# Kernel optimization log

Measured on AMD Instinct MI355X. Metric: run time of the kernel, lower is better.

## Reference

```python
import jax, jax.numpy as jnp
import numpy as np

HEADS = 16

def setup_inputs() -> dict:
    key = jax.random.key(0)
    ks = jax.random.split(key, 7)
    B, S, E = 2, 2048, 1024
    return {
        "query": jax.random.normal(ks[0], (B, S, E), dtype=jnp.float32),
        "key": jax.random.normal(ks[1], (B, S, E), dtype=jnp.float32),
        "value": jax.random.normal(ks[2], (B, S, E), dtype=jnp.float32),
        "Wqkv": jax.random.normal(ks[3], (E, 3 * E), dtype=jnp.float32) * (E ** -0.5),
        "bqkv": jax.random.normal(ks[4], (3 * E,), dtype=jnp.float32) * 0.02,
        "Wproj": jax.random.normal(ks[5], (E, E), dtype=jnp.float32) * (E ** -0.5),
        "bproj": jax.random.normal(ks[6], (E,), dtype=jnp.float32) * 0.02,
    }

def reference(query, key, value, Wqkv, bqkv, Wproj, bproj):
    # key/value args are unused in the original forward (overwritten by QKV split)
    B, S, E = query.shape
    H = HEADS
    hd = E // H
    qkv = query @ Wqkv + bqkv                     # [B, S, 3E]
    qkv = qkv.reshape(B, S, H, 3 * hd).transpose(0, 2, 1, 3)  # [B, H, S, 3hd]
    q = qkv[..., :hd]
    k = qkv[..., hd:2 * hd]
    v = qkv[..., 2 * hd:]
    qk = jnp.einsum("bhqd,bhkd->bhqk", q, k)
    # faithful quirk: original divides by head_dim**-0.5, i.e. multiplies by sqrt(hd)
    scaled = qk / (hd ** -0.5)
    attn = jax.nn.softmax(scaled, axis=-1)        # dropout p=0 -> identity
    out = jnp.einsum("bhqk,bhkd->bhqd", attn, v)  # [B, H, S, hd]
    out = out.transpose(0, 2, 1, 3).reshape(B, S, E)
    return out @ Wproj + bproj
```

## Files before the change

### kernel.cpp

```cpp
#include <hip/hip_runtime.h>
#include <hip/hip_bf16.h>
#include <stdint.h>

typedef __attribute__((ext_vector_type(8))) _Float16 f16x8;
typedef __attribute__((ext_vector_type(4))) _Float16 f16x4;
typedef __attribute__((ext_vector_type(4))) float f32x4;

static constexpr int BATCH = 2;
static constexpr int SEQ = 2048;
static constexpr int EMB = 1024;
static constexpr int NH = 16;
static constexpr int HD_ = 64;

#define AS1 __attribute__((address_space(1)))
#define AS3 __attribute__((address_space(3)))

__device__ __forceinline__ void gload_lds16(const void* g, void* l) {
  __builtin_amdgcn_global_load_lds((const AS1 uint32_t*)g, (AS3 uint32_t*)l, 16, 0, 0);
}

__device__ __forceinline__ f32x4 mfma16(f16x8 a, f16x8 b, f32x4 c) {
  return __builtin_amdgcn_mfma_f32_16x16x32_f16(a, b, c, 0, 0, 0);
}

__device__ __forceinline__ f16x8 swzread(const _Float16* base, int row, int blk) {
  return *(const f16x8*)((const char*)base + row * 128 +
                         ((blk * 16) ^ ((row & 7) << 4)));
}

__global__ __launch_bounds__(256) void k_prep(const float* __restrict__ q,
                                              _Float16* __restrict__ qo,
                                              const float* __restrict__ wqkv,
                                              _Float16* __restrict__ wqkvo,
                                              const float* __restrict__ wproj,
                                              _Float16* __restrict__ wprojo) {
  __shared__ float tile[32][33];
  const int blk = blockIdx.x;
  const int t = threadIdx.x;
  if (blk < 4096) {
    const int idx = blk * 256 + t;
    float4 v = reinterpret_cast<const float4*>(q)[idx];
    const float* f = reinterpret_cast<const float*>(&v);
    _Float16 h[4];
#pragma unroll
    for (int i = 0; i < 4; ++i) h[i] = (_Float16)f[i];
    reinterpret_cast<uint2*>(qo)[idx] = *reinterpret_cast<uint2*>(h);
    return;
  }
  const float* in;
  _Float16* out;
  int R, C, bx, by;
  bool perm;
  if (blk < 4096 + 3072) {
    const int lo = blk - 4096;
    bx = lo % 96;
    by = lo / 96;
    in = wqkv; out = wqkvo; R = 1024; C = 3072; perm = true;
  } else {
    const int lo = blk - 7168;
    bx = lo & 31;
    by = lo >> 5;
    in = wproj; out = wprojo; R = 1024; C = 1024; perm = false;
  }
  const int tr = t >> 5, tc = t & 31;
  const int r0 = by * 32, c0 = bx * 32;
#pragma unroll
  for (int rr = 0; rr < 32; rr += 8)
    tile[tr + rr][tc] = in[(size_t)(r0 + tr + rr) * C + c0 + tc];
  __syncthreads();
#pragma unroll
  for (int rr = 0; rr < 32; rr += 8) {
    const int c = c0 + tr + rr;
    int d = c;
    if (perm) {
      const int h = c / 192, r = c - h * 192;
      d = (r < 64) ? h * 64 + r
                   : (r < 128 ? 1024 + h * 64 + (r - 64) : 2048 + h * 64 + (r - 128));
    }
    out[(size_t)d * R + r0 + tc] = (_Float16)tile[tc][tr + rr];
  }
}

__global__ __launch_bounds__(256) void k_gemm_qkv(const _Float16* __restrict__ A,
                                                  const _Float16* __restrict__ Bt,
                                                  const float* __restrict__ bias,
                                                  _Float16* __restrict__ oq,
                                                  _Float16* __restrict__ ok,
                                                  _Float16* __restrict__ ov) {
  constexpr int K = EMB;
  __shared__ _Float16 As[2][128 * 32];
  __shared__ _Float16 Bs[2][128 * 32];
  const int t = threadIdx.x;
  const int l = t & 63, w = t >> 6;
  const int lr = l & 15, lg = l >> 4;
  const int wr = w >> 1, wc = w & 1;
  const int id = blockIdx.x;
  const int xcd = id & 7, wg = id >> 3;
  const int m0 = (xcd * 4 + wg / 24) * 128;
  const int n0 = (wg % 24) * 128;

  auto stage = [&](int buf, int k0) {
#pragma unroll
    for (int j = 0; j < 2; ++j) {
      const int c = t + 256 * j;
      const int row = c >> 2, cb = c & 3;
      gload_lds16(A + (size_t)(m0 + row) * K + k0 + cb * 8, &As[buf][c * 8]);
      gload_lds16(Bt + (size_t)(n0 + row) * K + k0 + cb * 8, &Bs[buf][c * 8]);
    }
  };

  f32x4 acc[4][4];
#pragma unroll
  for (int m = 0; m < 4; ++m)
#pragma unroll
    for (int n = 0; n < 4; ++n) acc[m][n] = f32x4{0.f, 0.f, 0.f, 0.f};

  stage(0, 0);
  const int NT = K / 32;
  int cur = 0;
  for (int kt = 0; kt < NT; ++kt) {
    __syncthreads();
    if (kt + 1 < NT) stage(cur ^ 1, (kt + 1) * 32);
    f16x8 af[4], bf[4];
#pragma unroll
    for (int m = 0; m < 4; ++m)
      af[m] = *(const f16x8*)&As[cur][(wr * 64 + m * 16 + lr) * 32 + lg * 8];
#pragma unroll
    for (int n = 0; n < 4; ++n)
      bf[n] = *(const f16x8*)&Bs[cur][(wc * 64 + n * 16 + lr) * 32 + lg * 8];
#pragma unroll
    for (int m = 0; m < 4; ++m)
#pragma unroll
      for (int n = 0; n < 4; ++n) acc[m][n] = mfma16(af[m], bf[n], acc[m][n]);
    cur ^= 1;
  }

  const int sec = n0 >> 10;
#pragma unroll
  for (int m = 0; m < 4; ++m) {
#pragma unroll
    for (int n = 0; n < 4; ++n) {
      const int col = n0 + wc * 64 + n * 16 + lr;
      const int cc = col & 1023;
      const int h = cc >> 6, r = cc & 63;
      const float bv = bias[h * 192 + sec * 64 + r];
      const int row0 = m0 + wr * 64 + m * 16 + lg * 4;
      const int b = row0 >> 11, s0 = row0 & (SEQ - 1);
      if (sec == 2) {
        f16x4 vv;
#pragma unroll
        for (int i = 0; i < 4; ++i) vv[i] = (_Float16)(acc[m][n][i] + bv);
        *(f16x4*)&ov[(((size_t)b * NH + h) * HD_ + r) * SEQ + s0] = vv;
      } else {
#pragma unroll
        for (int i = 0; i < 4; ++i) {
          const float v = acc[m][n][i] + bv;
          const size_t dst = (((size_t)b * NH + h) * SEQ + s0 + i) * HD_ + r;
          if (sec == 0)
            oq[dst] = (_Float16)(v * 11.5415603f);
          else
            ok[dst] = (_Float16)v;
        }
      }
    }
  }
}

__global__ __launch_bounds__(256) void k_gemm_proj(const _Float16* __restrict__ A,
                                                   const _Float16* __restrict__ Bt,
                                                   const float* __restrict__ bias,
                                                   float* __restrict__ of) {
  constexpr int K = EMB, N = EMB;
  __shared__ _Float16 As[2][128 * 32];
  __shared__ _Float16 Bs[2][128 * 32];
  const int t = threadIdx.x;
  const int l = t & 63, w = t >> 6;
  const int lr = l & 15, lg = l >> 4;
  const int wr = w >> 1, wc = w & 1;
  const int m0 = blockIdx.y * 128, n0 = blockIdx.x * 128;

  auto stage = [&](int buf, int k0) {
#pragma unroll
    for (int j = 0; j < 2; ++j) {
      const int c = t + 256 * j;
      const int row = c >> 2, cb = c & 3;
      gload_lds16(A + (size_t)(m0 + row) * K + k0 + cb * 8, &As[buf][c * 8]);
      gload_lds16(Bt + (size_t)(n0 + row) * K + k0 + cb * 8, &Bs[buf][c * 8]);
    }
  };

  f32x4 acc[4][4];
#pragma unroll
  for (int m = 0; m < 4; ++m)
#pragma unroll
    for (int n = 0; n < 4; ++n) acc[m][n] = f32x4{0.f, 0.f, 0.f, 0.f};

  stage(0, 0);
  const int NT = K / 32;
  int cur = 0;
  for (int kt = 0; kt < NT; ++kt) {
    __syncthreads();
    if (kt + 1 < NT) stage(cur ^ 1, (kt + 1) * 32);
    f16x8 af[4], bf[4];
#pragma unroll
    for (int m = 0; m < 4; ++m)
      af[m] = *(const f16x8*)&As[cur][(wr * 64 + m * 16 + lr) * 32 + lg * 8];
#pragma unroll
    for (int n = 0; n < 4; ++n)
      bf[n] = *(const f16x8*)&Bs[cur][(wc * 64 + n * 16 + lr) * 32 + lg * 8];
#pragma unroll
    for (int m = 0; m < 4; ++m)
#pragma unroll
      for (int n = 0; n < 4; ++n) acc[m][n] = mfma16(af[m], bf[n], acc[m][n]);
    cur ^= 1;
  }

#pragma unroll
  for (int m = 0; m < 4; ++m)
#pragma unroll
    for (int n = 0; n < 4; ++n)
#pragma unroll
      for (int i = 0; i < 4; ++i) {
        const int row = m0 + wr * 64 + m * 16 + lg * 4 + i;
        const int col = n0 + wc * 64 + n * 16 + lr;
        of[(size_t)row * N + col] = acc[m][n][i] + bias[col];
      }
}

__global__ __launch_bounds__(512) void k_attn(const _Float16* __restrict__ qs,
                                              const _Float16* __restrict__ ks,
                                              const _Float16* __restrict__ vt,
                                              _Float16* __restrict__ ao) {
  __shared__ _Float16 Kt[2][64][64];
  __shared__ _Float16 Vt[2][64][64];
  __shared__ _Float16 Plh[8][16][32];
  const int t = threadIdx.x;
  const int l = t & 63, w = t >> 6;
  const int lr = l & 15, lg = l >> 4;
  const int id = blockIdx.x;
  const int xc = id & 7, m_ = id >> 3;
  const int bh = xc + 8 * (m_ >> 4);
  const int qb = (m_ & 15) * 128 + w * 16;

  const size_t qoff = ((size_t)bh * SEQ + qb + lr) * HD_;
  const f16x8 qf0 = *(const f16x8*)(qs + qoff + lg * 8);
  const f16x8 qf1 = *(const f16x8*)(qs + qoff + 32 + lg * 8);

  const _Float16* kbase = ks + (size_t)bh * SEQ * HD_;
  const _Float16* vbase = vt + (size_t)bh * HD_ * SEQ;

  const int srow = t >> 3, scb = t & 7;
  auto stage = [&](const int buf, const int kv0) {
    gload_lds16(kbase + (size_t)(kv0 + srow) * HD_ + (scb ^ (srow & 7)) * 8,
                &Kt[buf][srow][scb * 8]);
    gload_lds16(vbase + (size_t)srow * SEQ + kv0 + (scb ^ (srow & 7)) * 8,
                &Vt[buf][srow][scb * 8]);
  };

  stage(0, 0);

  float mr = -1e30f, lsum = 0.f;
  f32x4 oacc[4];
#pragma unroll
  for (int n = 0; n < 4; ++n) oacc[n] = f32x4{0.f, 0.f, 0.f, 0.f};

  char* plbase = (char*)&Plh[w][0][0];
  const int plswz = ((lr >> 1) & 3) << 4;

  const int NT = SEQ / 64;
  for (int it = 0; it < NT; ++it) {
    const int cur = it & 1;
    __syncthreads();
    if (it + 1 < NT) stage(cur ^ 1, (it + 1) * 64);

    f32x4 sa[4];
    __builtin_amdgcn_s_setprio(1);
#pragma unroll
    for (int t4 = 0; t4 < 4; ++t4) {
      const int r = t4 * 16 + lr;
      const f16x8 kf0 = swzread(&Kt[cur][0][0], r, lg);
      const f16x8 kf1 = swzread(&Kt[cur][0][0], r, lg + 4);
      f32x4 s = mfma16(kf0, qf0, f32x4{0.f, 0.f, 0.f, 0.f});
      sa[t4] = mfma16(kf1, qf1, s);
    }
    __builtin_amdgcn_s_setprio(0);

    float t01 = fmaxf(fmaxf(sa[0][0], sa[0][1]), fmaxf(sa[0][2], sa[0][3]));
    float t23 = fmaxf(fmaxf(sa[1][0], sa[1][1]), fmaxf(sa[1][2], sa[1][3]));
    float t45 = fmaxf(fmaxf(sa[2][0], sa[2][1]), fmaxf(sa[2][2], sa[2][3]));
    float t67 = fmaxf(fmaxf(sa[3][0], sa[3][1]), fmaxf(sa[3][2], sa[3][3]));
    float tm = fmaxf(fmaxf(t01, t23), fmaxf(t45, t67));
    tm = fmaxf(tm, __shfl_xor(tm, 16));
    tm = fmaxf(tm, __shfl_xor(tm, 32));

    if (__all(tm < mr - 24.0f)) continue;

    if (__any(tm > mr + 8.0f)) {
      const float nm = fmaxf(mr, tm);
      const float corr = exp2f(mr - nm);
      mr = nm;
      lsum *= corr;
      float cb4[4];
#pragma unroll
      for (int i = 0; i < 4; ++i)
        cb4[i] = __shfl(corr, (l & 48) + ((l >> 4) << 2) + i);
#pragma unroll
      for (int n = 0; n < 4; ++n)
#pragma unroll
        for (int i = 0; i < 4; ++i) oacc[n][i] *= cb4[i];
    }

    float ts = 0.f;
#pragma unroll
    for (int H = 0; H < 2; ++H) {
#pragma unroll
      for (int th = 0; th < 2; ++th) {
        const int t4 = 2 * H + th;
        f16x4 pp;
#pragma unroll
        for (int i = 0; i < 4; ++i) {
          const float p = exp2f(sa[t4][i] - mr);
          ts += p;
          pp[i] = (_Float16)p;
        }
        *(f16x4*)(plbase + lr * 64 + ((th * 32 + lg * 8) ^ plswz)) = pp;
      }
      const f16x8 aP = *(const f16x8*)(plbase + lr * 64 + ((lg * 16) ^ plswz));
      __builtin_amdgcn_s_setprio(1);
#pragma unroll
      for (int n = 0; n < 4; ++n) {
        const int d = n * 16 + lr;
        const f16x8 bv = swzread(&Vt[cur][0][0], d, lg + 4 * H);
        oacc[n] = mfma16(aP, bv, oacc[n]);
      }
      __builtin_amdgcn_s_setprio(0);
    }
    ts += __shfl_xor(ts, 16);
    ts += __shfl_xor(ts, 32);
    lsum += ts;
  }

  float ls4[4];
#pragma unroll
  for (int i = 0; i < 4; ++i)
    ls4[i] = __shfl(lsum, (l & 48) + ((l >> 4) << 2) + i);
  const int b = bh >> 4, h = bh & 15;
#pragma unroll
  for (int n = 0; n < 4; ++n)
#pragma unroll
    for (int i = 0; i < 4; ++i) {
      const int row = qb + ((l >> 4) << 2) + i;
      ao[((size_t)b * SEQ + row) * EMB + h * HD_ + n * 16 + lr] =
          (_Float16)(oacc[n][i] / ls4[i]);
    }
}

extern "C" void kernel_launch(void* const* d_in, const int* in_sizes, int n_in,
                              void* d_out, int out_size, void* d_ws, size_t ws_size,
                              hipStream_t stream) {
  const float* query = (const float*)d_in[0];
  const float* Wqkv = (const float*)d_in[3];
  const float* bqkv = (const float*)d_in[4];
  const float* Wproj = (const float*)d_in[5];
  const float* bproj = (const float*)d_in[6];
  float* out = (float*)d_out;

  char* ws = (char*)d_ws;
  const size_t MB = 1024 * 1024;
  _Float16* q_f16   = (_Float16*)(ws + 0);
  _Float16* Wqkv_t  = (_Float16*)(ws + 16 * MB);
  _Float16* q_s     = (_Float16*)(ws + 24 * MB);
  _Float16* k_s     = (_Float16*)(ws + 32 * MB);
  _Float16* v_t     = (_Float16*)(ws + 40 * MB);
  _Float16* Wproj_t = (_Float16*)(ws + 48 * MB);
  _Float16* a_o     = (_Float16*)(ws + 51 * MB);

  const int M = BATCH * SEQ;
  k_prep<<<dim3(8192), 256, 0, stream>>>(query, q_f16, Wqkv, Wqkv_t, Wproj, Wproj_t);
  k_gemm_qkv<<<dim3(768), 256, 0, stream>>>(q_f16, Wqkv_t, bqkv, q_s, k_s, v_t);
  k_attn<<<dim3(512), 512, 0, stream>>>(q_s, k_s, v_t, a_o);
  k_gemm_proj<<<dim3(EMB / 128, M / 128), 256, 0, stream>>>(a_o, Wproj_t, bproj, out);
}
```

Before: 147.9 us.

## Remap GEMM tiles per XCD and restructure attention P staging into one pass

```diff
diff --git a/kernel.cpp b/kernel.cpp
--- a/kernel.cpp
+++ b/kernel.cpp
@@ -96,8 +96,10 @@
   const int wr = w >> 1, wc = w & 1;
   const int id = blockIdx.x;
   const int xcd = id & 7, wg = id >> 3;
-  const int m0 = (xcd * 4 + wg / 24) * 128;
-  const int n0 = (wg % 24) * 128;
+  const int mq = xcd & 3, ng = xcd >> 2;
+  const int mi = wg / 12, ni = wg % 12;
+  const int m0 = (mq * 8 + mi) * 128;
+  const int n0 = (ng * 12 + ni) * 128;
 
   auto stage = [&](int buf, int k0) {
 #pragma unroll
@@ -177,7 +179,10 @@
   const int l = t & 63, w = t >> 6;
   const int lr = l & 15, lg = l >> 4;
   const int wr = w >> 1, wc = w & 1;
-  const int m0 = blockIdx.y * 128, n0 = blockIdx.x * 128;
+  const int id = blockIdx.x;
+  const int xcd = id & 7, wg = id >> 3;
+  const int m0 = (xcd * 4 + wg / 8) * 128;
+  const int n0 = (wg & 7) * 128;
 
   auto stage = [&](int buf, int k0) {
 #pragma unroll
@@ -233,7 +238,7 @@
                                               _Float16* __restrict__ ao) {
   __shared__ _Float16 Kt[2][64][64];
   __shared__ _Float16 Vt[2][64][64];
-  __shared__ _Float16 Plh[8][16][32];
+  __shared__ _Float16 Pl[8][16][64];
   const int t = threadIdx.x;
   const int l = t & 63, w = t >> 6;
   const int lr = l & 15, lg = l >> 4;
@@ -264,9 +269,6 @@
 #pragma unroll
   for (int n = 0; n < 4; ++n) oacc[n] = f32x4{0.f, 0.f, 0.f, 0.f};
 
-  char* plbase = (char*)&Plh[w][0][0];
-  const int plswz = ((lr >> 1) & 3) << 4;
-
   const int NT = SEQ / 64;
   for (int it = 0; it < NT; ++it) {
     const int cur = it & 1;
@@ -311,33 +313,34 @@
     }
 
     float ts = 0.f;
-#pragma unroll
-    for (int H = 0; H < 2; ++H) {
-#pragma unroll
-      for (int th = 0; th < 2; ++th) {
-        const int t4 = 2 * H + th;
-        f16x4 pp;
-#pragma unroll
-        for (int i = 0; i < 4; ++i) {
-          const float p = exp2f(sa[t4][i] - mr);
-          ts += p;
-          pp[i] = (_Float16)p;
-        }
-        *(f16x4*)(plbase + lr * 64 + ((th * 32 + lg * 8) ^ plswz)) = pp;
+    char* plbase = (char*)&Pl[w][0][0];
+#pragma unroll
+    for (int t4 = 0; t4 < 4; ++t4) {
+      f16x4 pp;
+#pragma unroll
+      for (int i = 0; i < 4; ++i) {
+        const float p = exp2f(sa[t4][i] - mr);
+        ts += p;
+        pp[i] = (_Float16)p;
       }
-      const f16x8 aP = *(const f16x8*)(plbase + lr * 64 + ((lg * 16) ^ plswz));
-      __builtin_amdgcn_s_setprio(1);
-#pragma unroll
-      for (int n = 0; n < 4; ++n) {
-        const int d = n * 16 + lr;
-        const f16x8 bv = swzread(&Vt[cur][0][0], d, lg + 4 * H);
-        oacc[n] = mfma16(aP, bv, oacc[n]);
-      }
-      __builtin_amdgcn_s_setprio(0);
+      *(f16x4*)(plbase + lr * 128 + ((t4 * 32 + lg * 8) ^ ((lr & 7) << 4))) = pp;
     }
     ts += __shfl_xor(ts, 16);
     ts += __shfl_xor(ts, 32);
     lsum += ts;
+
+    const f16x8 aP0 = swzread(&Pl[w][0][0], lr, lg);
+    const f16x8 aP1 = swzread(&Pl[w][0][0], lr, lg + 4);
+    __builtin_amdgcn_s_setprio(1);
+#pragma unroll
+    for (int n = 0; n < 4; ++n) {
+      const int d = n * 16 + lr;
+      const f16x8 bv0 = swzread(&Vt[cur][0][0], d, lg);
+      const f16x8 bv1 = swzread(&Vt[cur][0][0], d, lg + 4);
+      oacc[n] = mfma16(aP0, bv0, oacc[n]);
+      oacc[n] = mfma16(aP1, bv1, oacc[n]);
+    }
+    __builtin_amdgcn_s_setprio(0);
   }
 
   float ls4[4];
@@ -379,5 +382,5 @@
   k_prep<<<dim3(8192), 256, 0, stream>>>(query, q_f16, Wqkv, Wqkv_t, Wproj, Wproj_t);
   k_gemm_qkv<<<dim3(768), 256, 0, stream>>>(q_f16, Wqkv_t, bqkv, q_s, k_s, v_t);
   k_attn<<<dim3(512), 512, 0, stream>>>(q_s, k_s, v_t, a_o);
-  k_gemm_proj<<<dim3(EMB / 128, M / 128), 256, 0, stream>>>(a_o, Wproj_t, bproj, out);
-}
+  k_gemm_proj<<<dim3(256), 256, 0, stream>>>(a_o, Wproj_t, bproj, out);
+}
```

Result: no change. 146.0 us (-1.3%).
